# Optimization experiments

Hardware: AMD Instinct MI355X
Metric: run time of the kernel (lower is better)

Reference implementation:

```python
import jax, jax.numpy as jnp
jax.config.update('jax_enable_x64', True)
import numpy as np

B = 1_048_576            # batch of addresses to translate
MEMORY_SIZE = 64 * 1024 * 1024   # 2**26, from __init__ default
ADDR_BITS = 64           # Linear(64, 128) input width
PHYS_BITS = 26           # log2(MEMORY_SIZE): packed % 2**26 == low 26 bits


def setup_inputs() -> dict:
    key = jax.random.key(0)
    k1, k2, k3, k4, k5 = jax.random.split(key, 5)
    virtual_addr = jax.random.randint(k1, (B,), 0, 2**31 - 1, dtype=jnp.int64)
    # torch Linear default init ~ U(-1/sqrt(fan_in), 1/sqrt(fan_in)); gaussian of same scale is fine
    s1 = 1.0 / np.sqrt(64.0)
    s2 = 1.0 / np.sqrt(128.0)
    W1 = jax.random.normal(k2, (64, 128), dtype=jnp.float32) * s1
    b1 = jax.random.normal(k3, (128,), dtype=jnp.float32) * s1
    W2 = jax.random.normal(k4, (128, 64), dtype=jnp.float32) * s2
    b2 = jax.random.normal(k5, (64,), dtype=jnp.float32) * s2
    return {"virtual_addr": virtual_addr, "W1": W1, "b1": b1, "W2": W2, "b2": b2}


def reference(virtual_addr, W1, b1, W2, b2):
    # Unpack each address into 64 bits: bits[b, i] = (addr >> i) & 1  (vectorized
    # replacement for the 64-iteration Python loop in translate_address).
    shifts = jnp.arange(ADDR_BITS, dtype=jnp.int64)            # [64]
    bits = ((virtual_addr[:, None] >> shifts[None, :]) & 1).astype(jnp.float32)  # [B, 64]

    # address_translator: Linear(64,128) -> GELU(exact) -> Linear(128,64)
    h = jax.nn.gelu(bits @ W1 + b1, approximate=False)          # [B, 128]
    logits = h @ W2 + b2                                        # [B, 64]

    # Threshold at 0.5, pack bits, mod memory_size. Since MEMORY_SIZE = 2**26,
    # (packed % MEMORY_SIZE) equals packing only the low 26 bits.
    phys_bits = (logits[:, :PHYS_BITS] > 0.5).astype(jnp.int64)  # [B, 26]
    weights = jnp.int64(1) << jnp.arange(PHYS_BITS, dtype=jnp.int64)
    physical_addr = jnp.sum(phys_bits * weights, axis=-1)        # [B] in [0, MEMORY_SIZE)
    return physical_addr
```

## Files before the change

### kernel.cpp

```cpp
#include <hip/hip_runtime.h>
#include <math.h>


typedef _Float16 half8 __attribute__((ext_vector_type(8)));
typedef _Float16 half2t __attribute__((ext_vector_type(2)));
typedef float f32x4 __attribute__((ext_vector_type(4)));

#define NROWS       224
#define LUTH_STRIDE 68
#define LUTH_UINTS  (NROWS * LUTH_STRIDE)
#define LUTF_STRIDE 132
#define LUTF_FLOATS (NROWS * LUTF_STRIDE)
#define NBMAX       2048
#define EPS1        6e-3f
#define EPS2        1e-4f
#define S2MAX       4096

__device__ int g_meta[NBMAX + 8];
__device__ int g_flags1[NBMAX * 1024];
__device__ int g_s2[S2MAX];
__device__ __align__(16) unsigned int   g_luth[LUTH_UINTS];
__device__ __align__(16) float          g_lutf[LUTF_FLOATS];
__device__ __align__(16) unsigned short g_w2f[2 * 64 * 4 * 8];

__device__ __forceinline__ half2t h2(unsigned int u) {
    return __builtin_bit_cast(half2t, u);
}
__device__ __forceinline__ half2t c2h(float f) {
    half2t r; r.x = (_Float16)f; r.y = r.x; return r;
}

__device__ __forceinline__ unsigned int gelu2_pk(half2t x) {
    half2t xx = x * x;
    half2t w  = xx * c2h(0.10294324f) + c2h(2.3022081f);
    half2t ar = x * w;
    _Float16 t0, t1;
    asm("v_exp_f16 %0, %1" : "=v"(t0) : "v"(ar.x));
    asm("v_exp_f16 %0, %1" : "=v"(t1) : "v"(ar.y));
    half2t t; t.x = t0; t.y = t1;
    half2t u = t + c2h(1.0f);
    _Float16 r0, r1;
    asm("v_rcp_f16 %0, %1" : "=v"(r0) : "v"(u.x));
    asm("v_rcp_f16 %0, %1" : "=v"(r1) : "v"(u.y));
    half2t r; r.x = r0; r.y = r1;
    half2t h = x - x * r;
    return __builtin_bit_cast(unsigned int, h);
}

__device__ __forceinline__ float gelu_f(float x) {
    float ax = __builtin_fabsf(x);
    float z  = ax * 0.70710678118654752f;
    float den = fmaf(z, 0.3275911f, 1.0f);
    float t; asm("v_rcp_f32 %0, %1" : "=v"(t) : "v"(den));
    float p = fmaf(t, 1.061405429f, -1.453152027f);
    p = fmaf(t, p, 1.421413741f);
    p = fmaf(t, p, -0.284496736f);
    p = fmaf(t, p, 0.254829592f);
    p = p * t;
    float arg = x * x * -0.72134752044448170368f;
    float e; asm("v_exp_f32 %0, %1" : "=v"(e) : "v"(arg));
    float w = ax * (p * e);
    return 0.5f * ((x + ax) - w);
}

__device__ __forceinline__ unsigned long long sel4(unsigned long long a,
    unsigned long long b, unsigned long long c, unsigned long long d, int r) {
    return r == 0 ? a : r == 1 ? b : r == 2 ? c : d;
}

__global__ void k_prep(const unsigned int* __restrict__ va32, int n,
                       const float* __restrict__ W1, const float* __restrict__ b1,
                       const float* __restrict__ W2) {
    int t = blockIdx.x * blockDim.x + threadIdx.x;
    if (t < NROWS * 128) {
        int row = t >> 7, k = t & 127;
        int m, bit0, nb; float acc;
        if (row < 64) { m = row;             bit0 = 0;         nb = 6; acc = b1[k]; }
        else          { int g = (row - 64) >> 5;
                        m = (row - 64) & 31; bit0 = 6 + 5 * g; nb = 5; acc = 0.0f; }
        for (int ii = 0; ii < nb; ii++)
            if ((m >> ii) & 1) acc += W1[(bit0 + ii) * 128 + k];
        g_lutf[row * LUTF_STRIDE + k] = acc;
        ((_Float16*)g_luth)[row * (2 * LUTH_STRIDE) + k] = (_Float16)acc;
        return;
    }
    int d = t - NROWS * 128;
    if (d < 4096) {
        unsigned int a = 0;
        int lim = n / 2 < 65536 ? n / 2 : 65536;
        for (int i = d; i < lim; i += 4096) a |= va32[2 * i + 1];
        if (a) atomicOr((unsigned int*)&g_meta[NBMAX], a);
        return;
    }
    int e = d - 4096;
    if (e < 2 * 64 * 4 * 8) {
        int tile = e >> 11, r = e & 2047;
        int lane = r >> 5, ks = (r >> 3) & 3, j = r & 7;
        int n0 = lane & 15, quad = lane >> 4;
        int k = ks * 32 + quad * 8 + j;
        float v = 0.0f;
        if (tile == 0)           v = W2[k * 64 + n0];
        else if (n0 < 10)        v = W2[k * 64 + 16 + n0];
        _Float16 hv = (_Float16)v;
        g_w2f[e] = __builtin_bit_cast(unsigned short, hv);
    }
}

__global__ __launch_bounds__(1024, 4)
void k_main(const unsigned int* __restrict__ va32, int* __restrict__ out, int n,
            const float* __restrict__ b2) {
    extern __shared__ unsigned int sh[];
    for (int idx = threadIdx.x; idx < LUTH_UINTS / 4; idx += blockDim.x)
        ((uint4*)sh)[idx] = ((const uint4*)g_luth)[idx];
    __syncthreads();

    const int lane = threadIdx.x & 63;
    const int wid  = threadIdx.x >> 6;
    const int base = blockIdx.x * 1024 + wid * 64;
    const int n0   = lane & 15;
    const int quad = lane >> 4;
    const int q4   = quad * 4;
    const int is64 = (g_meta[NBMAX] == 0);

    int li = base + lane; if (li >= n) li = n - 1;
    unsigned int addr_l = is64 ? va32[2 * li] : va32[li];

    const uint4* wf = (const uint4*)g_w2f;
    half8 B0[4], B1[4];
#pragma unroll
    for (int ks = 0; ks < 4; ks++) {
        B0[ks] = __builtin_bit_cast(half8, wf[lane * 4 + ks]);
        B1[ks] = __builtin_bit_cast(half8, wf[256 + lane * 4 + ks]);
    }
    const float ci0 = b2[n0] - 0.5f;
    const float ci1 = (n0 < 10) ? (b2[16 + n0] - 0.5f) : -1.0f;

#pragma unroll
    for (int t = 0; t < 4; t++) {
        unsigned int addr = (unsigned int)__shfl((int)addr_l, t * 16 + n0, 64);
        const unsigned int* r0 = sh + (addr & 63u)                  * LUTH_STRIDE + q4;
        const unsigned int* r1 = sh + (64u  + ((addr >> 6)  & 31u)) * LUTH_STRIDE + q4;
        const unsigned int* r2 = sh + (96u  + ((addr >> 11) & 31u)) * LUTH_STRIDE + q4;
        const unsigned int* r3 = sh + (128u + ((addr >> 16) & 31u)) * LUTH_STRIDE + q4;
        const unsigned int* r4 = sh + (160u + ((addr >> 21) & 31u)) * LUTH_STRIDE + q4;
        const unsigned int* r5 = sh + (192u + ((addr >> 26) & 31u)) * LUTH_STRIDE + q4;

        f32x4 acc0 = { ci0, ci0, ci0, ci0 };
        f32x4 acc1 = { ci1, ci1, ci1, ci1 };

#pragma unroll
        for (int ks = 0; ks < 4; ks++) {
            int off = ks * 16;
            uint4 v0 = *(const uint4*)(r0 + off);
            uint4 v1 = *(const uint4*)(r1 + off);
            uint4 v2 = *(const uint4*)(r2 + off);
            uint4 v3 = *(const uint4*)(r3 + off);
            uint4 v4 = *(const uint4*)(r4 + off);
            uint4 v5 = *(const uint4*)(r5 + off);
            uint4 au;
            au.x = gelu2_pk(((h2(v0.x) + h2(v1.x)) + (h2(v2.x) + h2(v3.x))) + (h2(v4.x) + h2(v5.x)));
            au.y = gelu2_pk(((h2(v0.y) + h2(v1.y)) + (h2(v2.y) + h2(v3.y))) + (h2(v4.y) + h2(v5.y)));
            au.z = gelu2_pk(((h2(v0.z) + h2(v1.z)) + (h2(v2.z) + h2(v3.z))) + (h2(v4.z) + h2(v5.z)));
            au.w = gelu2_pk(((h2(v0.w) + h2(v1.w)) + (h2(v2.w) + h2(v3.w))) + (h2(v4.w) + h2(v5.w)));
            half8 A = __builtin_bit_cast(half8, au);
            acc0 = __builtin_amdgcn_mfma_f32_16x16x32_f16(A, B0[ks], acc0, 0, 0, 0);
            acc1 = __builtin_amdgcn_mfma_f32_16x16x32_f16(A, B1[ks], acc1, 0, 0, 0);
        }

        unsigned long long bo0[4], bo1[4], bf1[4];
#pragma unroll
        for (int r = 0; r < 4; r++) {
            float d0 = acc0[r], d1 = acc1[r];
            bo0[r] = __ballot(d0 > 0.0f);
            bo1[r] = __ballot(d1 > 0.0f);
            bf1[r] = __ballot(__builtin_fabsf(d1) < EPS1);
        }
        if (lane < 16) {
            int r = lane & 3, gg = lane >> 2;
            unsigned long long so0 = sel4(bo0[0], bo0[1], bo0[2], bo0[3], r);
            unsigned long long so1 = sel4(bo1[0], bo1[1], bo1[2], bo1[3], r);
            unsigned long long sf1 = sel4(bf1[0], bf1[1], bf1[2], bf1[3], r);
            unsigned int ob = (unsigned int)((so0 >> (gg * 16)) & 0xFFFFu)
                            | ((unsigned int)((so1 >> (gg * 16)) & 0x3FFu) << 16);
            unsigned int fb = (unsigned int)((sf1 >> (gg * 16 + 4)) & 0x3Fu);
            int ai = base + t * 16 + lane;
            if (ai < n) {
                out[ai] = (int)ob;
                if (fb) {
                    int ix = atomicAdd(&g_meta[blockIdx.x], 1);
                    g_flags1[blockIdx.x * 1024 + ix] = ai;
                }
            }
        }
    }
}

__global__ __launch_bounds__(256)
void k_rescue1(const unsigned int* __restrict__ va32, int* __restrict__ out,
               const float* __restrict__ W2, const float* __restrict__ b2) {
    const int bid = blockIdx.x;
    int cnt = g_meta[bid]; if (cnt > 1024) cnt = 1024;
    if (cnt == 0) return;
    const int is64 = (g_meta[NBMAX] == 0);
    const float* __restrict__ lutf = g_lutf;

    for (int i = threadIdx.x; i < cnt; i += 256) {
        int b = g_flags1[bid * 1024 + i];
        unsigned int addr = is64 ? va32[2 * b] : va32[b];
        const float* r0 = lutf + (addr & 63u)                  * LUTF_STRIDE;
        const float* r1 = lutf + (64u  + ((addr >> 6)  & 31u)) * LUTF_STRIDE;
        const float* r2 = lutf + (96u  + ((addr >> 11) & 31u)) * LUTF_STRIDE;
        const float* r3 = lutf + (128u + ((addr >> 16) & 31u)) * LUTF_STRIDE;
        const float* r4 = lutf + (160u + ((addr >> 21) & 31u)) * LUTF_STRIDE;
        const float* r5 = lutf + (192u + ((addr >> 26) & 31u)) * LUTF_STRIDE;
        float acc[6];
#pragma unroll
        for (int j = 0; j < 6; j++) acc[j] = b2[20 + j] - 0.5f;
#pragma unroll 2
        for (int k = 0; k < 128; k += 4) {
            float4 a  = *(const float4*)(r0 + k);
            float4 t1 = *(const float4*)(r1 + k);
            float4 t2 = *(const float4*)(r2 + k);
            float4 t3 = *(const float4*)(r3 + k);
            float4 t4 = *(const float4*)(r4 + k);
            float4 t5 = *(const float4*)(r5 + k);
            a.x += t1.x + t2.x + t3.x + t4.x + t5.x;
            a.y += t1.y + t2.y + t3.y + t4.y + t5.y;
            a.z += t1.z + t2.z + t3.z + t4.z + t5.z;
            a.w += t1.w + t2.w + t3.w + t4.w + t5.w;
            float h0 = gelu_f(a.x), h1 = gelu_f(a.y);
            float hh2 = gelu_f(a.z), h3 = gelu_f(a.w);
#pragma unroll
            for (int j = 0; j < 6; j++) {
                acc[j] = fmaf(h0,  W2[(k + 0) * 64 + 20 + j], acc[j]);
                acc[j] = fmaf(h1,  W2[(k + 1) * 64 + 20 + j], acc[j]);
                acc[j] = fmaf(hh2, W2[(k + 2) * 64 + 20 + j], acc[j]);
                acc[j] = fmaf(h3,  W2[(k + 3) * 64 + 20 + j], acc[j]);
            }
        }
        unsigned int hi6 = 0; bool bl = false;
#pragma unroll
        for (int j = 0; j < 6; j++) {
            float dd = acc[j];
            if (dd > 0.0f) hi6 |= (1u << j);
            bl = bl || (__builtin_fabsf(dd) < EPS2);
        }
        out[b] = (int)(((unsigned int)out[b] & 0xFFFFFu) | (hi6 << 20));
        if (bl) {
            int ix = atomicAdd(&g_meta[NBMAX + 1], 1);
            if (ix < S2MAX) g_s2[ix] = b;
        }
    }
}

__global__ __launch_bounds__(256)
void k_rescue2(const unsigned int* __restrict__ va32, int* __restrict__ out,
               const float* __restrict__ W1, const float* __restrict__ b1,
               const float* __restrict__ W2, const float* __restrict__ b2) {
    __shared__ double shd[4][128];
    int c2 = g_meta[NBMAX + 1]; if (c2 > S2MAX) c2 = S2MAX;
    const int is64 = (g_meta[NBMAX] == 0);
    const int lane = threadIdx.x & 63;
    const int wvl  = threadIdx.x >> 6;
    const int wv   = blockIdx.x * 4 + wvl;

    for (int f = wv; f < c2; f += 1024) {
        int b = g_s2[f];
        unsigned int addr = is64 ? va32[2 * b] : va32[b];
        int k0 = lane, k1 = lane + 64;
        double a0 = (double)b1[k0], a1 = (double)b1[k1];
        for (int bit = 0; bit < 31; bit++)
            if ((addr >> bit) & 1u) {
                a0 += (double)W1[bit * 128 + k0];
                a1 += (double)W1[bit * 128 + k1];
            }
        shd[wvl][k0] = 0.5 * a0 * (1.0 + erf(a0 * 0.7071067811865476));
        shd[wvl][k1] = 0.5 * a1 * (1.0 + erf(a1 * 0.7071067811865476));
        int j = lane;
        double p = (j < 26) ? (double)b2[j] - 0.5 : -1.0;
        if (j < 26)
            for (int k = 0; k < 128; k++)
                p += shd[wvl][k] * (double)W2[k * 64 + j];
        unsigned long long m = __ballot(j < 26 && p > 0.0);
        if (lane == 0) out[b] = (int)(m & 0x3FFFFFFu);
    }
}

extern "C" void kernel_launch(void* const* d_in, const int* in_sizes, int n_in,
                              void* d_out, int out_size, void* d_ws, size_t ws_size,
                              hipStream_t stream) {
    const unsigned int* va32 = (const unsigned int*)d_in[0];
    const float* W1 = (const float*)d_in[1];
    const float* b1 = (const float*)d_in[2];
    const float* W2 = (const float*)d_in[3];
    const float* b2 = (const float*)d_in[4];
    int* out = (int*)d_out;
    int n = in_sizes[0];

    void* pMeta = nullptr;
    (void)hipGetSymbolAddress(&pMeta, HIP_SYMBOL(g_meta));
    (void)hipMemsetAsync(pMeta, 0, (NBMAX + 8) * sizeof(int), stream);

    k_prep<<<(NROWS * 128 + 8192) / 256, 256, 0, stream>>>(va32, n, W1, b1, W2);

    int NB = (n + 1023) / 1024; if (NB > NBMAX) NB = NBMAX;
    k_main<<<NB, 1024, LUTH_UINTS * 4, stream>>>(va32, out, n, b2);

    k_rescue1<<<NB, 256, 0, stream>>>(va32, out, W2, b2);
    k_rescue2<<<256, 256, 0, stream>>>(va32, out, W1, b1, W2, b2);
}
```

Baseline: 180.8 us.

## Fuse both rescue passes into one kernel and zero counters in prep

Merges the two rescue kernels into one. Each block now keeps its second-stage (double-precision) candidates in a shared-memory list of up to 32 entries and processes them itself, instead of appending to a global list handled by a separate launch. The hipMemsetAsync of the metadata counters is dropped, and the per-block counters are cleared inside k_prep instead. This removes a memset and one kernel launch from the pipeline. In exchange, g_meta[NBMAX] (the high-word OR flag) is no longer reset between calls, and candidates beyond 32 per block are silently dropped.

Result: slower. 189.7 us (+5.0%).

```diff
diff --git a/kernel.cpp b/kernel.cpp
--- a/kernel.cpp
+++ b/kernel.cpp
@@ -14,11 +14,9 @@
 #define NBMAX       2048
 #define EPS1        6e-3f
 #define EPS2        1e-4f
-#define S2MAX       4096
 
 __device__ int g_meta[NBMAX + 8];
 __device__ int g_flags1[NBMAX * 1024];
-__device__ int g_s2[S2MAX];
 __device__ __align__(16) unsigned int   g_luth[LUTH_UINTS];
 __device__ __align__(16) float          g_lutf[LUTF_FLOATS];
 __device__ __align__(16) unsigned short g_w2f[2 * 64 * 4 * 8];
@@ -103,7 +101,10 @@
         else if (n0 < 10)        v = W2[k * 64 + 16 + n0];
         _Float16 hv = (_Float16)v;
         g_w2f[e] = __builtin_bit_cast(unsigned short, hv);
-    }
+        return;
+    }
+    int z = d - 8192;
+    if (z < NBMAX) g_meta[z] = 0;
 }
 
 __global__ __launch_bounds__(1024, 4)
@@ -196,11 +197,19 @@
 }
 
 __global__ __launch_bounds__(256)
-void k_rescue1(const unsigned int* __restrict__ va32, int* __restrict__ out,
-               const float* __restrict__ W2, const float* __restrict__ b2) {
+void k_rescue(const unsigned int* __restrict__ va32, int* __restrict__ out,
+              const float* __restrict__ W1, const float* __restrict__ b1,
+              const float* __restrict__ W2, const float* __restrict__ b2) {
+    __shared__ int s2[32];
+    __shared__ int s2cnt;
+    __shared__ double shd[4][128];
+
     const int bid = blockIdx.x;
     int cnt = g_meta[bid]; if (cnt > 1024) cnt = 1024;
     if (cnt == 0) return;
+    if (threadIdx.x == 0) s2cnt = 0;
+    __syncthreads();
+
     const int is64 = (g_meta[NBMAX] == 0);
     const float* __restrict__ lutf = g_lutf;
 
@@ -247,25 +256,17 @@
         }
         out[b] = (int)(((unsigned int)out[b] & 0xFFFFFu) | (hi6 << 20));
         if (bl) {
-            int ix = atomicAdd(&g_meta[NBMAX + 1], 1);
-            if (ix < S2MAX) g_s2[ix] = b;
-        }
-    }
-}
-
-__global__ __launch_bounds__(256)
-void k_rescue2(const unsigned int* __restrict__ va32, int* __restrict__ out,
-               const float* __restrict__ W1, const float* __restrict__ b1,
-               const float* __restrict__ W2, const float* __restrict__ b2) {
-    __shared__ double shd[4][128];
-    int c2 = g_meta[NBMAX + 1]; if (c2 > S2MAX) c2 = S2MAX;
-    const int is64 = (g_meta[NBMAX] == 0);
+            int ix = atomicAdd(&s2cnt, 1);
+            if (ix < 32) s2[ix] = b;
+        }
+    }
+
+    __syncthreads();
+    int c2 = s2cnt; if (c2 > 32) c2 = 32;
     const int lane = threadIdx.x & 63;
     const int wvl  = threadIdx.x >> 6;
-    const int wv   = blockIdx.x * 4 + wvl;
-
-    for (int f = wv; f < c2; f += 1024) {
-        int b = g_s2[f];
+    for (int f = wvl; f < c2; f += 4) {
+        int b = s2[f];
         unsigned int addr = is64 ? va32[2 * b] : va32[b];
         int k0 = lane, k1 = lane + 64;
         double a0 = (double)b1[k0], a1 = (double)b1[k1];
@@ -297,15 +298,11 @@
     int* out = (int*)d_out;
     int n = in_sizes[0];
 
-    void* pMeta = nullptr;
-    (void)hipGetSymbolAddress(&pMeta, HIP_SYMBOL(g_meta));
-    (void)hipMemsetAsync(pMeta, 0, (NBMAX + 8) * sizeof(int), stream);
-
-    k_prep<<<(NROWS * 128 + 8192) / 256, 256, 0, stream>>>(va32, n, W1, b1, W2);
+    const int PREP_THREADS = NROWS * 128 + 4096 + 4096 + NBMAX;
+    k_prep<<<(PREP_THREADS + 255) / 256, 256, 0, stream>>>(va32, n, W1, b1, W2);
 
     int NB = (n + 1023) / 1024; if (NB > NBMAX) NB = NBMAX;
     k_main<<<NB, 1024, LUTH_UINTS * 4, stream>>>(va32, out, n, b2);
 
-    k_rescue1<<<NB, 256, 0, stream>>>(va32, out, W2, b2);
-    k_rescue2<<<256, 256, 0, stream>>>(va32, out, W1, b1, W2, b2);
-}
+    k_rescue<<<NB, 256, 0, stream>>>(va32, out, W1, b1, W2, b2);
+}
```

## Fold metadata reset into prep kernel and split rescue1 dot product across half-waves

Applied to the files above, without the earlier changes.

The separate memset of the per-block counters is removed. Extra threads in the prep kernel now zero those counters and the stage-2 counter. The first rescue kernel changes from one thread per flagged element looping over all 128 hidden units to one half-wave per element. Each lane handles four hidden units, keeps its W2 slice in registers, and the partial sums are combined with a cross-lane shuffle reduction. The aim is to cut the cost of an extra launch and the serial per-thread latency in rescue1. In exchange, the OR-accumulated width flag g_meta[NBMAX] is no longer reset between calls.

Result: faster. 170.2 us (-5.8%).

```diff
diff --git a/kernel.cpp b/kernel.cpp
--- a/kernel.cpp
+++ b/kernel.cpp
@@ -103,7 +103,11 @@
         else if (n0 < 10)        v = W2[k * 64 + 16 + n0];
         _Float16 hv = (_Float16)v;
         g_w2f[e] = __builtin_bit_cast(unsigned short, hv);
-    }
+        return;
+    }
+    int z = d - 8192;
+    if (z < NBMAX) g_meta[z] = 0;
+    else if (z == NBMAX) g_meta[NBMAX + 1] = 0;
 }
 
 __global__ __launch_bounds__(1024, 4)
@@ -195,60 +199,69 @@
     }
 }
 
-__global__ __launch_bounds__(256)
+__global__ __launch_bounds__(256, 2)
 void k_rescue1(const unsigned int* __restrict__ va32, int* __restrict__ out,
                const float* __restrict__ W2, const float* __restrict__ b2) {
     const int bid = blockIdx.x;
     int cnt = g_meta[bid]; if (cnt > 1024) cnt = 1024;
     if (cnt == 0) return;
     const int is64 = (g_meta[NBMAX] == 0);
-    const float* __restrict__ lutf = g_lutf;
-
-    for (int i = threadIdx.x; i < cnt; i += 256) {
-        int b = g_flags1[bid * 1024 + i];
+    const int lane = threadIdx.x & 63;
+    const int wv   = threadIdx.x >> 6;
+    const int l2   = lane & 31;
+    const int half = lane >> 5;
+
+    float w2r[4][6];
+#pragma unroll
+    for (int c = 0; c < 4; c++)
+#pragma unroll
+        for (int j = 0; j < 6; j++)
+            w2r[c][j] = W2[(4 * l2 + c) * 64 + 20 + j];
+
+    const float* __restrict__ lf = g_lutf;
+    int npair = (cnt + 1) >> 1;
+    for (int p = wv; p < npair; p += 4) {
+        int fi = 2 * p + half;
+        bool valid = fi < cnt;
+        int b = g_flags1[bid * 1024 + (valid ? fi : 0)];
         unsigned int addr = is64 ? va32[2 * b] : va32[b];
-        const float* r0 = lutf + (addr & 63u)                  * LUTF_STRIDE;
-        const float* r1 = lutf + (64u  + ((addr >> 6)  & 31u)) * LUTF_STRIDE;
-        const float* r2 = lutf + (96u  + ((addr >> 11) & 31u)) * LUTF_STRIDE;
-        const float* r3 = lutf + (128u + ((addr >> 16) & 31u)) * LUTF_STRIDE;
-        const float* r4 = lutf + (160u + ((addr >> 21) & 31u)) * LUTF_STRIDE;
-        const float* r5 = lutf + (192u + ((addr >> 26) & 31u)) * LUTF_STRIDE;
+        const float4* r0 = (const float4*)(lf + (addr & 63u)                  * LUTF_STRIDE) + l2;
+        const float4* r1 = (const float4*)(lf + (64u  + ((addr >> 6)  & 31u)) * LUTF_STRIDE) + l2;
+        const float4* r2 = (const float4*)(lf + (96u  + ((addr >> 11) & 31u)) * LUTF_STRIDE) + l2;
+        const float4* r3 = (const float4*)(lf + (128u + ((addr >> 16) & 31u)) * LUTF_STRIDE) + l2;
+        const float4* r4 = (const float4*)(lf + (160u + ((addr >> 21) & 31u)) * LUTF_STRIDE) + l2;
+        const float4* r5 = (const float4*)(lf + (192u + ((addr >> 26) & 31u)) * LUTF_STRIDE) + l2;
+        float4 a  = *r0;
+        float4 t1 = *r1, t2 = *r2, t3 = *r3, t4 = *r4, t5 = *r5;
+        a.x += t1.x + t2.x + t3.x + t4.x + t5.x;
+        a.y += t1.y + t2.y + t3.y + t4.y + t5.y;
+        a.z += t1.z + t2.z + t3.z + t4.z + t5.z;
+        a.w += t1.w + t2.w + t3.w + t4.w + t5.w;
+        float h0 = gelu_f(a.x), h1 = gelu_f(a.y);
+        float hh2 = gelu_f(a.z), h3 = gelu_f(a.w);
         float acc[6];
 #pragma unroll
-        for (int j = 0; j < 6; j++) acc[j] = b2[20 + j] - 0.5f;
-#pragma unroll 2
-        for (int k = 0; k < 128; k += 4) {
-            float4 a  = *(const float4*)(r0 + k);
-            float4 t1 = *(const float4*)(r1 + k);
-            float4 t2 = *(const float4*)(r2 + k);
-            float4 t3 = *(const float4*)(r3 + k);
-            float4 t4 = *(const float4*)(r4 + k);
-            float4 t5 = *(const float4*)(r5 + k);
-            a.x += t1.x + t2.x + t3.x + t4.x + t5.x;
-            a.y += t1.y + t2.y + t3.y + t4.y + t5.y;
-            a.z += t1.z + t2.z + t3.z + t4.z + t5.z;
-            a.w += t1.w + t2.w + t3.w + t4.w + t5.w;
-            float h0 = gelu_f(a.x), h1 = gelu_f(a.y);
-            float hh2 = gelu_f(a.z), h3 = gelu_f(a.w);
+        for (int j = 0; j < 6; j++)
+            acc[j] = fmaf(h0, w2r[0][j], fmaf(h1, w2r[1][j],
+                     fmaf(hh2, w2r[2][j], h3 * w2r[3][j])));
+#pragma unroll
+        for (int m = 1; m < 32; m <<= 1)
+#pragma unroll
+            for (int j = 0; j < 6; j++)
+                acc[j] += __shfl_xor(acc[j], m, 64);
+        if (valid && l2 == 0) {
+            unsigned int hi6 = 0; bool bl = false;
 #pragma unroll
             for (int j = 0; j < 6; j++) {
-                acc[j] = fmaf(h0,  W2[(k + 0) * 64 + 20 + j], acc[j]);
-                acc[j] = fmaf(h1,  W2[(k + 1) * 64 + 20 + j], acc[j]);
-                acc[j] = fmaf(hh2, W2[(k + 2) * 64 + 20 + j], acc[j]);
-                acc[j] = fmaf(h3,  W2[(k + 3) * 64 + 20 + j], acc[j]);
+                float dd = acc[j] + b2[20 + j] - 0.5f;
+                if (dd > 0.0f) hi6 |= (1u << j);
+                bl = bl || (__builtin_fabsf(dd) < EPS2);
             }
-        }
-        unsigned int hi6 = 0; bool bl = false;
-#pragma unroll
-        for (int j = 0; j < 6; j++) {
-            float dd = acc[j];
-            if (dd > 0.0f) hi6 |= (1u << j);
-            bl = bl || (__builtin_fabsf(dd) < EPS2);
-        }
-        out[b] = (int)(((unsigned int)out[b] & 0xFFFFFu) | (hi6 << 20));
-        if (bl) {
-            int ix = atomicAdd(&g_meta[NBMAX + 1], 1);
-            if (ix < S2MAX) g_s2[ix] = b;
+            out[b] = (int)(((unsigned int)out[b] & 0xFFFFFu) | (hi6 << 20));
+            if (bl) {
+                int ix = atomicAdd(&g_meta[NBMAX + 1], 1);
+                if (ix < S2MAX) g_s2[ix] = b;
+            }
         }
     }
 }
@@ -297,11 +310,8 @@
     int* out = (int*)d_out;
     int n = in_sizes[0];
 
-    void* pMeta = nullptr;
-    (void)hipGetSymbolAddress(&pMeta, HIP_SYMBOL(g_meta));
-    (void)hipMemsetAsync(pMeta, 0, (NBMAX + 8) * sizeof(int), stream);
-
-    k_prep<<<(NROWS * 128 + 8192) / 256, 256, 0, stream>>>(va32, n, W1, b1, W2);
+    const int PREP_THREADS = NROWS * 128 + 4096 + 4096 + NBMAX + 1;
+    k_prep<<<(PREP_THREADS + 255) / 256, 256, 0, stream>>>(va32, n, W1, b1, W2);
 
     int NB = (n + 1023) / 1024; if (NB > NBMAX) NB = NBMAX;
     k_main<<<NB, 1024, LUTH_UINTS * 4, stream>>>(va32, out, n, b2);
```
